# Optimization experiments

Measured on AMD Instinct MI355X. Metric: run time of the kernel, lower is better.

Reference implementation:

```python
import jax, jax.numpy as jnp
import numpy as np

N = 100000      # nodes (dtype==2 subgraph)
E = 1600000     # edges
IN_DIM = 256
OUT_DIM = 64
FEAT_DIM = 64   # hard-coded by nn.Linear(64, out_dim) in dstfeat_fc


def setup_inputs() -> dict:
    key = jax.random.key(0)
    k1, k2, k3, k4, k5, k6 = jax.random.split(key, 6)
    h = jax.random.normal(k1, (N, IN_DIM), dtype=jnp.float32)
    feat = jax.random.normal(k2, (N, FEAT_DIM), dtype=jnp.float32)
    W_fc = jax.random.normal(k3, (OUT_DIM, IN_DIM), dtype=jnp.float32) * 0.05
    W_dst = jax.random.normal(k4, (OUT_DIM, FEAT_DIM), dtype=jnp.float32) * 0.05
    src = jax.random.randint(k5, (E,), 0, N, dtype=jnp.int64)
    dst = jax.random.randint(k6, (E,), 0, N, dtype=jnp.int64)
    return {"h": h, "feat": feat, "W_fc": W_fc, "W_dst": W_dst, "src": src, "dst": dst}


def reference(h, feat, W_fc, W_dst, src, dst):
    # node projections (done once per node, then gathered per edge)
    z = h @ W_fc.T            # [N, OUT]  (self.fc)
    df = feat @ W_dst.T       # [N, OUT]  (self.dstfeat_fc on dst 'feat')

    # per-edge attention logit: dot(z[src], dstfeat[dst])
    e = jnp.sum(z[src] * df[dst], axis=-1)          # [E]

    # segment softmax over incoming edges of each destination node
    emax = jax.ops.segment_max(e, dst, num_segments=N)
    emax = jnp.where(jnp.isfinite(emax), emax, 0.0)  # guard empty segments
    ex = jnp.exp(e - emax[dst])                      # [E]
    denom = jax.ops.segment_sum(ex, dst, num_segments=N)  # [N]

    # weighted neighbor aggregation: sum_e alpha_e * z[src_e] per dst
    num = jax.ops.segment_sum(ex[:, None] * z[src], dst, num_segments=N)  # [N, OUT]
    out = num / jnp.where(denom == 0, 1.0, denom)[:, None]
    return out
```

## Files before the change

### kernel.cpp

```cpp
#include <hip/hip_runtime.h>
#include <math.h>

typedef unsigned int uint32;
typedef __attribute__((ext_vector_type(8))) short bf16x8;
typedef __attribute__((ext_vector_type(4))) float f32x4;

__device__ __forceinline__ ushort f2bf(float f) {
  uint32 u = __builtin_bit_cast(uint32, f);
  uint32 r = (u + 0x7fff + ((u >> 16) & 1)) >> 16;
  return (ushort)r;
}
__device__ __forceinline__ float bf_lo(uint32 u) {
  return __builtin_bit_cast(float, u << 16);
}
__device__ __forceinline__ float bf_hi(uint32 u) {
  return __builtin_bit_cast(float, u & 0xffff0000u);
}

template <bool BF16OUT>
__global__ __launch_bounds__(256) void gemm_mfma(const float* __restrict__ A,
                                                 const float* __restrict__ W,
                                                 float* __restrict__ C,
                                                 ushort* __restrict__ Cb,
                                                 int M, int K) {
  __shared__ __align__(16) ushort Ws[64 * 264];
  __shared__ __align__(16) ushort As[128 * 40];
  const int t = threadIdx.x;
  const int lane = t & 63;
  const int w = t >> 6;
  const int quad = lane >> 4;
  const int l16 = lane & 15;
  const int rBase = blockIdx.x * 128;

  const int kq4 = K >> 2;
  for (int idx = t; idx < 64 * kq4; idx += 256) {
    int row = idx / kq4, kq = idx - row * kq4;
    float4 v = *(const float4*)(W + (size_t)row * K + kq * 4);
    ushort4 b;
    b.x = f2bf(v.x); b.y = f2bf(v.y); b.z = f2bf(v.z); b.w = f2bf(v.w);
    *(ushort4*)&Ws[row * 264 + kq * 4] = b;
  }

  f32x4 acc[2][4];
  #pragma unroll
  for (int i = 0; i < 2; ++i)
    #pragma unroll
    for (int n = 0; n < 4; ++n) acc[i][n] = (f32x4){0.f, 0.f, 0.f, 0.f};

  const int rStage = t >> 1;
  const int halfStage = t & 1;

  for (int kb = 0; kb < K; kb += 32) {
    {
      int gr = rBase + rStage;
      #pragma unroll
      for (int q = 0; q < 4; ++q) {
        int kk = kb + halfStage * 16 + q * 4;
        float4 v = make_float4(0.f, 0.f, 0.f, 0.f);
        if (gr < M) v = *(const float4*)(A + (size_t)gr * K + kk);
        ushort4 b;
        b.x = f2bf(v.x); b.y = f2bf(v.y); b.z = f2bf(v.z); b.w = f2bf(v.w);
        *(ushort4*)&As[rStage * 40 + halfStage * 16 + q * 4] = b;
      }
    }
    __syncthreads();

    bf16x8 afrag[2], bfrag[4];
    #pragma unroll
    for (int i = 0; i < 2; ++i)
      afrag[i] = *(const bf16x8*)&As[(w * 32 + i * 16 + l16) * 40 + quad * 8];
    #pragma unroll
    for (int n = 0; n < 4; ++n)
      bfrag[n] = *(const bf16x8*)&Ws[(n * 16 + l16) * 264 + kb + quad * 8];

    #pragma unroll
    for (int i = 0; i < 2; ++i)
      #pragma unroll
      for (int n = 0; n < 4; ++n)
        acc[i][n] = __builtin_amdgcn_mfma_f32_16x16x32_bf16(afrag[i], bfrag[n],
                                                            acc[i][n], 0, 0, 0);
    __syncthreads();
  }

  #pragma unroll
  for (int i = 0; i < 2; ++i)
    #pragma unroll
    for (int nt = 0; nt < 4; ++nt)
      #pragma unroll
      for (int r = 0; r < 4; ++r) {
        int row = rBase + w * 32 + i * 16 + quad * 4 + r;
        int col = nt * 16 + l16;
        if (row < M) {
          if (BF16OUT)
            Cb[(size_t)row * 64 + col] = f2bf(acc[i][nt][r]);
          else
            C[(size_t)row * 64 + col] = acc[i][nt][r];
        }
      }
}

#define BBITS 7
#define BNODES 128
#define P_CHUNK 16384
#define P3_CAP 6144
#define MAXB 1024

__global__ __launch_bounds__(256) void bucket_count(const int* __restrict__ dst,
                                                    int* __restrict__ bucketCnt,
                                                    int E, int B) {
  __shared__ int lcnt[MAXB];
  const int t = threadIdx.x;
  for (int i = t; i < B; i += 256) lcnt[i] = 0;
  __syncthreads();
  int c0 = blockIdx.x * P_CHUNK, c1 = min(c0 + P_CHUNK, E);
  for (int i = c0 + t; i < c1; i += 256) atomicAdd(&lcnt[dst[i] >> BBITS], 1);
  __syncthreads();
  for (int b = t; b < B; b += 256) {
    int c = lcnt[b];
    if (c) atomicAdd(&bucketCnt[b], c);
  }
}

__global__ __launch_bounds__(1024) void bucket_scan(const int* __restrict__ bucketCnt,
                                                    int* __restrict__ bucketBase,
                                                    int* __restrict__ bucketCursor,
                                                    int* __restrict__ offsets,
                                                    int B, int N, int E) {
  __shared__ int waveSums[16];
  const int t = threadIdx.x;
  const int lane = t & 63, wave = t >> 6;
  int x = (t < B) ? bucketCnt[t] : 0;
  int inc = x;
  #pragma unroll
  for (int d = 1; d < 64; d <<= 1) {
    int o = __shfl_up(inc, d, 64);
    if (lane >= d) inc += o;
  }
  if (lane == 63) waveSums[wave] = inc;
  __syncthreads();
  int wbase = 0;
  #pragma unroll
  for (int w = 0; w < 16; ++w)
    if (w < wave) wbase += waveSums[w];
  int excl = wbase + inc - x;
  if (t < B) {
    bucketBase[t] = excl;
    bucketCursor[t] = excl;
  }
  if (t == 0) {
    bucketBase[B] = E;
    offsets[N] = E;
  }
}

__global__ __launch_bounds__(256) void bucket_partition(const int* __restrict__ src,
                                                        const int* __restrict__ dst,
                                                        int* __restrict__ bucketCursor,
                                                        unsigned* __restrict__ packed,
                                                        int E, int B) {
  __shared__ int lcnt[MAXB];
  __shared__ int lbase[MAXB];
  const int t = threadIdx.x;
  for (int i = t; i < B; i += 256) lcnt[i] = 0;
  __syncthreads();
  int c0 = blockIdx.x * P_CHUNK, c1 = min(c0 + P_CHUNK, E);
  for (int i = c0 + t; i < c1; i += 256) atomicAdd(&lcnt[dst[i] >> BBITS], 1);
  __syncthreads();
  for (int b = t; b < B; b += 256) {
    int c = lcnt[b];
    lbase[b] = c ? atomicAdd(&bucketCursor[b], c) : 0;
  }
  __syncthreads();
  for (int i = c0 + t; i < c1; i += 256) {
    int dv = dst[i];
    int b = dv >> BBITS;
    int pos = atomicAdd(&lbase[b], 1);
    packed[pos] = ((unsigned)src[i] << BBITS) | (unsigned)(dv & (BNODES - 1));
  }
}

__global__ __launch_bounds__(256) void bucket_finalize(const int* __restrict__ bucketBase,
                                                       unsigned* __restrict__ packed,
                                                       int* __restrict__ offsets, int N) {
  __shared__ unsigned stage[P3_CAP];
  __shared__ int cnt[BNODES];
  const int b = blockIdx.x;
  const int t = threadIdx.x;
  const int base = bucketBase[b];
  int n = bucketBase[b + 1] - base;
  if (n > P3_CAP) n = P3_CAP;
  for (int i = t; i < n; i += 256) stage[i] = packed[base + i];
  if (t < BNODES) cnt[t] = 0;
  __syncthreads();
  for (int i = t; i < n; i += 256) atomicAdd(&cnt[stage[i] & (BNODES - 1)], 1);
  __syncthreads();
  if (t < 64) {
    int cA = cnt[2 * t], cB = cnt[2 * t + 1];
    int s = cA + cB;
    int inc = s;
    #pragma unroll
    for (int d = 1; d < 64; d <<= 1) {
      int o = __shfl_up(inc, d, 64);
      if (t >= d) inc += o;
    }
    int excl = inc - s;
    cnt[2 * t] = base + excl;
    cnt[2 * t + 1] = base + excl + cA;
  }
  __syncthreads();
  const int node0 = b << BBITS;
  if (t < BNODES) {
    int g = node0 + t;
    if (g < N) offsets[g] = cnt[t];
  }
  __syncthreads();
  for (int i = t; i < n; i += 256) {
    unsigned v = stage[i];
    int pos = atomicAdd(&cnt[v & (BNODES - 1)], 1);
    packed[pos] = v >> BBITS;
  }
}

__global__ __launch_bounds__(256) void aggregate(const ushort* __restrict__ zb,
                                                 const float* __restrict__ df,
                                                 const int* __restrict__ offsets,
                                                 const int* __restrict__ edgeSrc,
                                                 float* __restrict__ out, int N) {
  int gwave = (blockIdx.x * blockDim.x + threadIdx.x) >> 6;
  int lane = threadIdx.x & 63;
  if (gwave >= N) return;
  const int d = __builtin_amdgcn_readfirstlane(gwave);
  const int g = lane >> 4;
  const int l16 = lane & 15;
  const int beg = offsets[d];
  const int end = offsets[d + 1];

  const float4 df4 = *(const float4*)(df + (size_t)d * 64 + l16 * 4);

  float m = -INFINITY, l = 0.f;
  float ax = 0.f, ay = 0.f, az = 0.f, aw = 0.f;

  for (int j0 = beg; j0 < end; j0 += 32) {
    const int nst = min(8, (end - j0 + 3) >> 2);
    uint2 zf[8];
    float ew[8];
    float bm = -INFINITY;

    #pragma unroll
    for (int st = 0; st < 8; ++st) {
      if (st < nst) {
        const int eidx = j0 + st * 4 + g;
        const bool act = eidx < end;
        int s = 0;
        if (act) s = edgeSrc[eidx];
        zf[st] = *(const uint2*)(zb + (size_t)s * 64 + l16 * 4);
        float p = bf_lo(zf[st].x) * df4.x;
        p = fmaf(bf_hi(zf[st].x), df4.y, p);
        p = fmaf(bf_lo(zf[st].y), df4.z, p);
        p = fmaf(bf_hi(zf[st].y), df4.w, p);
        p += __shfl_xor(p, 1, 64);
        p += __shfl_xor(p, 2, 64);
        p += __shfl_xor(p, 4, 64);
        p += __shfl_xor(p, 8, 64);
        ew[st] = act ? p : -INFINITY;
        bm = fmaxf(bm, ew[st]);
      }
    }
    bm = fmaxf(bm, __shfl_xor(bm, 16, 64));
    bm = fmaxf(bm, __shfl_xor(bm, 32, 64));

    const float nm = fmaxf(m, bm);
    const float alpha = __expf(m - nm);
    float sw = 0.f;
    #pragma unroll
    for (int st = 0; st < 8; ++st) {
      if (st < nst) {
        const float w = __expf(ew[st] - nm);
        ew[st] = w;
        sw += w;
      }
    }
    sw += __shfl_xor(sw, 16, 64);
    sw += __shfl_xor(sw, 32, 64);
    l = l * alpha + sw;
    m = nm;

    ax *= alpha; ay *= alpha; az *= alpha; aw *= alpha;
    #pragma unroll
    for (int st = 0; st < 8; ++st) {
      if (st < nst) {
        const float w = ew[st];
        ax = fmaf(w, bf_lo(zf[st].x), ax);
        ay = fmaf(w, bf_hi(zf[st].x), ay);
        az = fmaf(w, bf_lo(zf[st].y), az);
        aw = fmaf(w, bf_hi(zf[st].y), aw);
      }
    }
  }

  ax += __shfl_xor(ax, 16, 64); ax += __shfl_xor(ax, 32, 64);
  ay += __shfl_xor(ay, 16, 64); ay += __shfl_xor(ay, 32, 64);
  az += __shfl_xor(az, 16, 64); az += __shfl_xor(az, 32, 64);
  aw += __shfl_xor(aw, 16, 64); aw += __shfl_xor(aw, 32, 64);

  if (lane < 16) {
    const float inv = (l > 0.f) ? (1.f / l) : 0.f;
    float4 o;
    o.x = ax * inv; o.y = ay * inv; o.z = az * inv; o.w = aw * inv;
    *(float4*)(out + (size_t)d * 64 + l16 * 4) = o;
  }
}

extern "C" void kernel_launch(void* const* d_in, const int* in_sizes, int n_in,
                              void* d_out, int out_size, void* d_ws, size_t ws_size,
                              hipStream_t stream) {
  const float* h     = (const float*)d_in[0];
  const float* feat  = (const float*)d_in[1];
  const float* W_fc  = (const float*)d_in[2];
  const float* W_dst = (const float*)d_in[3];
  const int*   src   = (const int*)d_in[4];
  const int*   dst   = (const int*)d_in[5];
  float* out = (float*)d_out;

  const int N = in_sizes[1] / 64;
  const int E = in_sizes[4];
  const int IN_DIM = in_sizes[0] / N;
  const int FEAT_DIM = 64;
  const int B = (N + BNODES - 1) >> BBITS;

  char* ws = (char*)d_ws;
  ushort* zb = (ushort*)ws;
  float* df = (float*)(zb + (size_t)N * 64);
  int* offsets = (int*)(df + (size_t)N * 64);
  unsigned* packed = (unsigned*)(offsets + N + 1);
  int* bucketCnt = (int*)(packed + E);
  int* bucketBase = bucketCnt + B;
  int* bucketCursor = bucketBase + B + 1;

  hipMemsetAsync(bucketCnt, 0, sizeof(int) * (size_t)B, stream);

  int ggrid = (N + 127) / 128;
  gemm_mfma<true><<<ggrid, 256, 0, stream>>>(h, W_fc, nullptr, zb, N, IN_DIM);
  gemm_mfma<false><<<ggrid, 256, 0, stream>>>(feat, W_dst, df, nullptr, N, FEAT_DIM);

  int pgrid = (E + P_CHUNK - 1) / P_CHUNK;
  bucket_count<<<pgrid, 256, 0, stream>>>(dst, bucketCnt, E, B);
  bucket_scan<<<1, 1024, 0, stream>>>(bucketCnt, bucketBase, bucketCursor, offsets, B, N, E);
  bucket_partition<<<pgrid, 256, 0, stream>>>(src, dst, bucketCursor, packed, E, B);
  bucket_finalize<<<B, 256, 0, stream>>>(bucketBase, packed, offsets, N);

  aggregate<<<(N + 3) / 4, 256, 0, stream>>>(zb, df, offsets, (const int*)packed, out, N);
}
```

Baseline: 406.5 us.

## Replace two-level bucket sort CSR build with per-node atomic counting sort

Replaces the bucketed two-pass partition and finalize with a direct counting sort: global per-node degree atomics, a hierarchical three-kernel prefix scan, and a scatter that uses per-node atomic cursors. This drops the LDS staging and the second packed pass, but it puts 1.6M random global atomics in each of two kernels. It also adds kernel launches, and the order of edges within a node becomes nondeterministic. scan_top assumes nparts is at most 256.

```diff
diff --git a/kernel.cpp b/kernel.cpp
--- a/kernel.cpp
+++ b/kernel.cpp
@@ -99,126 +99,118 @@
       }
 }
 
-#define BBITS 7
-#define BNODES 128
-#define P_CHUNK 16384
-#define P3_CAP 6144
-#define MAXB 1024
-
-__global__ __launch_bounds__(256) void bucket_count(const int* __restrict__ dst,
-                                                    int* __restrict__ bucketCnt,
-                                                    int E, int B) {
-  __shared__ int lcnt[MAXB];
-  const int t = threadIdx.x;
-  for (int i = t; i < B; i += 256) lcnt[i] = 0;
-  __syncthreads();
-  int c0 = blockIdx.x * P_CHUNK, c1 = min(c0 + P_CHUNK, E);
-  for (int i = c0 + t; i < c1; i += 256) atomicAdd(&lcnt[dst[i] >> BBITS], 1);
-  __syncthreads();
-  for (int b = t; b < B; b += 256) {
-    int c = lcnt[b];
-    if (c) atomicAdd(&bucketCnt[b], c);
-  }
-}
-
-__global__ __launch_bounds__(1024) void bucket_scan(const int* __restrict__ bucketCnt,
-                                                    int* __restrict__ bucketBase,
-                                                    int* __restrict__ bucketCursor,
-                                                    int* __restrict__ offsets,
-                                                    int B, int N, int E) {
-  __shared__ int waveSums[16];
+__global__ __launch_bounds__(256) void deg_count(const int* __restrict__ dst,
+                                                 int* __restrict__ deg, int E) {
+  const int tid = blockIdx.x * blockDim.x + threadIdx.x;
+  const int stride = gridDim.x * blockDim.x;
+  const int E4 = E >> 2;
+  const int4* __restrict__ d4 = (const int4*)dst;
+  for (int i = tid; i < E4; i += stride) {
+    int4 v = d4[i];
+    atomicAdd(&deg[v.x], 1);
+    atomicAdd(&deg[v.y], 1);
+    atomicAdd(&deg[v.z], 1);
+    atomicAdd(&deg[v.w], 1);
+  }
+  for (int i = E4 * 4 + tid; i < E; i += stride) atomicAdd(&deg[dst[i]], 1);
+}
+
+__global__ __launch_bounds__(256) void scan_part(const int* __restrict__ deg,
+                                                 int* __restrict__ offsets,
+                                                 int* __restrict__ partials, int N) {
+  __shared__ int wsum[4];
   const int t = threadIdx.x;
   const int lane = t & 63, wave = t >> 6;
-  int x = (t < B) ? bucketCnt[t] : 0;
-  int inc = x;
+  const int i0 = blockIdx.x * 1024 + t * 4;
+  int v[4];
+  if (i0 + 3 < N) {
+    int4 x = *(const int4*)(deg + i0);
+    v[0] = x.x; v[1] = x.y; v[2] = x.z; v[3] = x.w;
+  } else {
+    #pragma unroll
+    for (int k = 0; k < 4; ++k) v[k] = (i0 + k < N) ? deg[i0 + k] : 0;
+  }
+  int s = v[0] + v[1] + v[2] + v[3];
+  int inc = s;
   #pragma unroll
   for (int d = 1; d < 64; d <<= 1) {
     int o = __shfl_up(inc, d, 64);
     if (lane >= d) inc += o;
   }
-  if (lane == 63) waveSums[wave] = inc;
+  if (lane == 63) wsum[wave] = inc;
   __syncthreads();
   int wbase = 0;
   #pragma unroll
-  for (int w = 0; w < 16; ++w)
-    if (w < wave) wbase += waveSums[w];
-  int excl = wbase + inc - x;
-  if (t < B) {
-    bucketBase[t] = excl;
-    bucketCursor[t] = excl;
-  }
-  if (t == 0) {
-    bucketBase[B] = E;
-    offsets[N] = E;
-  }
-}
-
-__global__ __launch_bounds__(256) void bucket_partition(const int* __restrict__ src,
-                                                        const int* __restrict__ dst,
-                                                        int* __restrict__ bucketCursor,
-                                                        unsigned* __restrict__ packed,
-                                                        int E, int B) {
-  __shared__ int lcnt[MAXB];
-  __shared__ int lbase[MAXB];
+  for (int w = 0; w < 4; ++w)
+    if (w < wave) wbase += wsum[w];
+  int run = wbase + inc - s;
+  if (i0 + 3 < N) {
+    int4 o;
+    o.x = run; o.y = run + v[0]; o.z = run + v[0] + v[1]; o.w = run + v[0] + v[1] + v[2];
+    *(int4*)(offsets + i0) = o;
+  } else {
+    #pragma unroll
+    for (int k = 0; k < 4; ++k) {
+      if (i0 + k < N) offsets[i0 + k] = run;
+      run += v[k];
+    }
+  }
+  if (t == 255) partials[blockIdx.x] = wbase + inc;
+}
+
+__global__ __launch_bounds__(256) void scan_top(int* __restrict__ partials,
+                                                int* __restrict__ offsets,
+                                                int nparts, int N, int E) {
+  __shared__ int wsum[4];
   const int t = threadIdx.x;
-  for (int i = t; i < B; i += 256) lcnt[i] = 0;
+  const int lane = t & 63, wave = t >> 6;
+  int x = (t < nparts) ? partials[t] : 0;
+  int inc = x;
+  #pragma unroll
+  for (int d = 1; d < 64; d <<= 1) {
+    int o = __shfl_up(inc, d, 64);
+    if (lane >= d) inc += o;
+  }
+  if (lane == 63) wsum[wave] = inc;
   __syncthreads();
-  int c0 = blockIdx.x * P_CHUNK, c1 = min(c0 + P_CHUNK, E);
-  for (int i = c0 + t; i < c1; i += 256) atomicAdd(&lcnt[dst[i] >> BBITS], 1);
-  __syncthreads();
-  for (int b = t; b < B; b += 256) {
-    int c = lcnt[b];
-    lbase[b] = c ? atomicAdd(&bucketCursor[b], c) : 0;
-  }
-  __syncthreads();
-  for (int i = c0 + t; i < c1; i += 256) {
-    int dv = dst[i];
-    int b = dv >> BBITS;
-    int pos = atomicAdd(&lbase[b], 1);
-    packed[pos] = ((unsigned)src[i] << BBITS) | (unsigned)(dv & (BNODES - 1));
-  }
-}
-
-__global__ __launch_bounds__(256) void bucket_finalize(const int* __restrict__ bucketBase,
-                                                       unsigned* __restrict__ packed,
-                                                       int* __restrict__ offsets, int N) {
-  __shared__ unsigned stage[P3_CAP];
-  __shared__ int cnt[BNODES];
-  const int b = blockIdx.x;
-  const int t = threadIdx.x;
-  const int base = bucketBase[b];
-  int n = bucketBase[b + 1] - base;
-  if (n > P3_CAP) n = P3_CAP;
-  for (int i = t; i < n; i += 256) stage[i] = packed[base + i];
-  if (t < BNODES) cnt[t] = 0;
-  __syncthreads();
-  for (int i = t; i < n; i += 256) atomicAdd(&cnt[stage[i] & (BNODES - 1)], 1);
-  __syncthreads();
-  if (t < 64) {
-    int cA = cnt[2 * t], cB = cnt[2 * t + 1];
-    int s = cA + cB;
-    int inc = s;
-    #pragma unroll
-    for (int d = 1; d < 64; d <<= 1) {
-      int o = __shfl_up(inc, d, 64);
-      if (t >= d) inc += o;
-    }
-    int excl = inc - s;
-    cnt[2 * t] = base + excl;
-    cnt[2 * t + 1] = base + excl + cA;
-  }
-  __syncthreads();
-  const int node0 = b << BBITS;
-  if (t < BNODES) {
-    int g = node0 + t;
-    if (g < N) offsets[g] = cnt[t];
-  }
-  __syncthreads();
-  for (int i = t; i < n; i += 256) {
-    unsigned v = stage[i];
-    int pos = atomicAdd(&cnt[v & (BNODES - 1)], 1);
-    packed[pos] = v >> BBITS;
-  }
+  int wbase = 0;
+  #pragma unroll
+  for (int w = 0; w < 4; ++w)
+    if (w < wave) wbase += wsum[w];
+  if (t < nparts) partials[t] = wbase + inc - x;
+  if (t == 0) offsets[N] = E;
+}
+
+__global__ __launch_bounds__(256) void scan_add(int* __restrict__ offsets,
+                                                const int* __restrict__ partials,
+                                                int* __restrict__ cursor, int N) {
+  const int i = blockIdx.x * blockDim.x + threadIdx.x;
+  if (i < N) {
+    int v = offsets[i] + partials[i >> 10];
+    offsets[i] = v;
+    cursor[i] = v;
+  }
+}
+
+__global__ __launch_bounds__(256) void scatter(const int* __restrict__ src,
+                                               const int* __restrict__ dst,
+                                               int* __restrict__ cursor,
+                                               int* __restrict__ edgeSrc, int E) {
+  const int tid = blockIdx.x * blockDim.x + threadIdx.x;
+  const int stride = gridDim.x * blockDim.x;
+  const int E4 = E >> 2;
+  const int4* __restrict__ d4 = (const int4*)dst;
+  const int4* __restrict__ s4 = (const int4*)src;
+  for (int i = tid; i < E4; i += stride) {
+    int4 dv = d4[i];
+    int4 sv = s4[i];
+    edgeSrc[atomicAdd(&cursor[dv.x], 1)] = sv.x;
+    edgeSrc[atomicAdd(&cursor[dv.y], 1)] = sv.y;
+    edgeSrc[atomicAdd(&cursor[dv.z], 1)] = sv.z;
+    edgeSrc[atomicAdd(&cursor[dv.w], 1)] = sv.w;
+  }
+  for (int i = E4 * 4 + tid; i < E; i += stride)
+    edgeSrc[atomicAdd(&cursor[dst[i]], 1)] = src[i];
 }
 
 __global__ __launch_bounds__(256) void aggregate(const ushort* __restrict__ zb,
@@ -325,29 +317,27 @@
   const int N = in_sizes[1] / 64;
   const int E = in_sizes[4];
   const int IN_DIM = in_sizes[0] / N;
-  const int FEAT_DIM = 64;
-  const int B = (N + BNODES - 1) >> BBITS;
 
   char* ws = (char*)d_ws;
   ushort* zb = (ushort*)ws;
   float* df = (float*)(zb + (size_t)N * 64);
-  int* offsets = (int*)(df + (size_t)N * 64);
-  unsigned* packed = (unsigned*)(offsets + N + 1);
-  int* bucketCnt = (int*)(packed + E);
-  int* bucketBase = bucketCnt + B;
-  int* bucketCursor = bucketBase + B + 1;
-
-  hipMemsetAsync(bucketCnt, 0, sizeof(int) * (size_t)B, stream);
+  int* deg = (int*)(df + (size_t)N * 64);
+  int* offsets = deg + N;
+  int* edgeSrc = offsets + N + 1;
+  int* partials = edgeSrc + E;
+
+  hipMemsetAsync(deg, 0, sizeof(int) * (size_t)N, stream);
 
   int ggrid = (N + 127) / 128;
   gemm_mfma<true><<<ggrid, 256, 0, stream>>>(h, W_fc, nullptr, zb, N, IN_DIM);
-  gemm_mfma<false><<<ggrid, 256, 0, stream>>>(feat, W_dst, df, nullptr, N, FEAT_DIM);
-
-  int pgrid = (E + P_CHUNK - 1) / P_CHUNK;
-  bucket_count<<<pgrid, 256, 0, stream>>>(dst, bucketCnt, E, B);
-  bucket_scan<<<1, 1024, 0, stream>>>(bucketCnt, bucketBase, bucketCursor, offsets, B, N, E);
-  bucket_partition<<<pgrid, 256, 0, stream>>>(src, dst, bucketCursor, packed, E, B);
-  bucket_finalize<<<B, 256, 0, stream>>>(bucketBase, packed, offsets, N);
-
-  aggregate<<<(N + 3) / 4, 256, 0, stream>>>(zb, df, offsets, (const int*)packed, out, N);
-}
+  gemm_mfma<false><<<ggrid, 256, 0, stream>>>(feat, W_dst, df, nullptr, N, 64);
+
+  const int nparts = (N + 1023) / 1024;
+  deg_count<<<1024, 256, 0, stream>>>(dst, deg, E);
+  scan_part<<<nparts, 256, 0, stream>>>(deg, offsets, partials, N);
+  scan_top<<<1, 256, 0, stream>>>(partials, offsets, nparts, N, E);
+  scan_add<<<(N + 255) / 256, 256, 0, stream>>>(offsets, partials, deg, N);
+  scatter<<<1024, 256, 0, stream>>>(src, dst, deg, edgeSrc, E);
+
+  aggregate<<<(N + 3) / 4, 256, 0, stream>>>(zb, df, offsets, edgeSrc, out, N);
+}
```

Measured after the change: 480.0 us. 18.1% more time.

## Replace single-pass bucket partition with coarse-then-fine two-level radix partition

Applied to the files above, without the earlier changes.

The CSR build now partitions edges by destination in two levels. A first pass scatters into about 49 coarse buckets, a middle pass splits each coarse bucket into 16 fine buckets, and a finalize pass sorts within each node. This replaces the single scatter into roughly 782 buckets, which had poorly coalesced writes and heavy global atomic traffic. It also uses smaller chunks (2048 edges) so more blocks run in parallel, and borrows the output buffer as scratch. The cost is an extra kernel launch and an extra full pass over the edge array.

```diff
diff --git a/kernel.cpp b/kernel.cpp
--- a/kernel.cpp
+++ b/kernel.cpp
@@ -99,37 +99,41 @@
       }
 }
 
-#define BBITS 7
-#define BNODES 128
-#define P_CHUNK 16384
+#define FBITS 7
+#define FNODES 128
+#define CBITS 11
+#define CH 2048
+#define S4_CAP 4096
 #define P3_CAP 6144
-#define MAXB 1024
-
-__global__ __launch_bounds__(256) void bucket_count(const int* __restrict__ dst,
-                                                    int* __restrict__ bucketCnt,
-                                                    int E, int B) {
-  __shared__ int lcnt[MAXB];
-  const int t = threadIdx.x;
-  for (int i = t; i < B; i += 256) lcnt[i] = 0;
-  __syncthreads();
-  int c0 = blockIdx.x * P_CHUNK, c1 = min(c0 + P_CHUNK, E);
-  for (int i = c0 + t; i < c1; i += 256) atomicAdd(&lcnt[dst[i] >> BBITS], 1);
-  __syncthreads();
-  for (int b = t; b < B; b += 256) {
+
+__global__ __launch_bounds__(256) void fine_count(const int* __restrict__ dst,
+                                                  int* __restrict__ fineCnt,
+                                                  int E, int Bf) {
+  __shared__ int lcnt[1024];
+  const int t = threadIdx.x;
+  for (int i = t; i < Bf; i += 256) lcnt[i] = 0;
+  __syncthreads();
+  int c0 = blockIdx.x * CH, c1 = min(c0 + CH, E);
+  for (int i = c0 + t; i < c1; i += 256) atomicAdd(&lcnt[dst[i] >> FBITS], 1);
+  __syncthreads();
+  for (int b = t; b < Bf; b += 256) {
     int c = lcnt[b];
-    if (c) atomicAdd(&bucketCnt[b], c);
-  }
-}
-
-__global__ __launch_bounds__(1024) void bucket_scan(const int* __restrict__ bucketCnt,
-                                                    int* __restrict__ bucketBase,
-                                                    int* __restrict__ bucketCursor,
-                                                    int* __restrict__ offsets,
-                                                    int B, int N, int E) {
+    if (c) atomicAdd(&fineCnt[b], c);
+  }
+}
+
+__global__ __launch_bounds__(1024) void scan_fine(const int* __restrict__ fineCnt,
+                                                  int* __restrict__ fineBase,
+                                                  int* __restrict__ fineCursor,
+                                                  int* __restrict__ coarseBase,
+                                                  int* __restrict__ coarseCursor,
+                                                  int* __restrict__ offsets,
+                                                  int Bf, int NC, int N, int E) {
   __shared__ int waveSums[16];
+  __shared__ int sExcl[1024];
   const int t = threadIdx.x;
   const int lane = t & 63, wave = t >> 6;
-  int x = (t < B) ? bucketCnt[t] : 0;
+  int x = (t < Bf) ? fineCnt[t] : 0;
   int inc = x;
   #pragma unroll
   for (int d = 1; d < 64; d <<= 1) {
@@ -143,56 +147,106 @@
   for (int w = 0; w < 16; ++w)
     if (w < wave) wbase += waveSums[w];
   int excl = wbase + inc - x;
-  if (t < B) {
-    bucketBase[t] = excl;
-    bucketCursor[t] = excl;
+  sExcl[t] = excl;
+  if (t < Bf) {
+    fineBase[t] = excl;
+    fineCursor[t] = excl;
   }
   if (t == 0) {
-    bucketBase[B] = E;
+    fineBase[Bf] = E;
     offsets[N] = E;
-  }
-}
-
-__global__ __launch_bounds__(256) void bucket_partition(const int* __restrict__ src,
+    coarseBase[NC] = E;
+  }
+  __syncthreads();
+  if (t < NC) {
+    int v = sExcl[t * 16];
+    coarseBase[t] = v;
+    coarseCursor[t] = v;
+  }
+}
+
+__global__ __launch_bounds__(256) void coarse_partition(const int* __restrict__ src,
                                                         const int* __restrict__ dst,
-                                                        int* __restrict__ bucketCursor,
-                                                        unsigned* __restrict__ packed,
-                                                        int E, int B) {
-  __shared__ int lcnt[MAXB];
-  __shared__ int lbase[MAXB];
-  const int t = threadIdx.x;
-  for (int i = t; i < B; i += 256) lcnt[i] = 0;
-  __syncthreads();
-  int c0 = blockIdx.x * P_CHUNK, c1 = min(c0 + P_CHUNK, E);
-  for (int i = c0 + t; i < c1; i += 256) atomicAdd(&lcnt[dst[i] >> BBITS], 1);
-  __syncthreads();
-  for (int b = t; b < B; b += 256) {
-    int c = lcnt[b];
-    lbase[b] = c ? atomicAdd(&bucketCursor[b], c) : 0;
+                                                        int* __restrict__ coarseCursor,
+                                                        unsigned* __restrict__ packedA,
+                                                        int E, int NC) {
+  __shared__ int lcnt[64];
+  __shared__ int lbase[64];
+  const int t = threadIdx.x;
+  if (t < NC) lcnt[t] = 0;
+  __syncthreads();
+  int c0 = blockIdx.x * CH, c1 = min(c0 + CH, E);
+  for (int i = c0 + t; i < c1; i += 256) atomicAdd(&lcnt[dst[i] >> CBITS], 1);
+  __syncthreads();
+  if (t < NC) {
+    int c = lcnt[t];
+    lbase[t] = c ? atomicAdd(&coarseCursor[t], c) : 0;
   }
   __syncthreads();
   for (int i = c0 + t; i < c1; i += 256) {
     int dv = dst[i];
-    int b = dv >> BBITS;
+    int b = dv >> CBITS;
     int pos = atomicAdd(&lbase[b], 1);
-    packed[pos] = ((unsigned)src[i] << BBITS) | (unsigned)(dv & (BNODES - 1));
-  }
-}
-
-__global__ __launch_bounds__(256) void bucket_finalize(const int* __restrict__ bucketBase,
-                                                       unsigned* __restrict__ packed,
-                                                       int* __restrict__ offsets, int N) {
+    packedA[pos] = ((unsigned)src[i] << CBITS) | (unsigned)(dv & ((1 << CBITS) - 1));
+  }
+}
+
+__global__ __launch_bounds__(256) void mid_partition(const unsigned* __restrict__ packedA,
+                                                     const int* __restrict__ coarseBase,
+                                                     int* __restrict__ fineCursor,
+                                                     unsigned* __restrict__ packedB) {
+  __shared__ unsigned stage[S4_CAP];
+  __shared__ int cnt[16];
+  __shared__ int lbase[16];
+  const int cb = blockIdx.x >> 4;
+  const int sub = blockIdx.x & 15;
+  const int t = threadIdx.x;
+  const int base = coarseBase[cb];
+  const int endr = coarseBase[cb + 1];
+  const int len = endr - base;
+  const int chunk = (len + 15) >> 4;
+  int s0 = base + sub * chunk;
+  int s1 = min(s0 + chunk, endr);
+  for (int p0 = s0; p0 < s1; p0 += S4_CAP) {
+    const int n = min(S4_CAP, s1 - p0);
+    if (t < 16) cnt[t] = 0;
+    __syncthreads();
+    for (int i = t; i < n; i += 256) {
+      unsigned v = packedA[p0 + i];
+      stage[i] = v;
+      atomicAdd(&cnt[(v >> FBITS) & 15], 1);
+    }
+    __syncthreads();
+    if (t < 16) {
+      int c = cnt[t];
+      lbase[t] = c ? atomicAdd(&fineCursor[cb * 16 + t], c) : 0;
+    }
+    __syncthreads();
+    for (int i = t; i < n; i += 256) {
+      unsigned v = stage[i];
+      int f = (v >> FBITS) & 15;
+      int pos = atomicAdd(&lbase[f], 1);
+      packedB[pos] = ((v >> CBITS) << FBITS) | (v & (FNODES - 1));
+    }
+    __syncthreads();
+  }
+}
+
+__global__ __launch_bounds__(256) void fine_finalize(const int* __restrict__ fineBase,
+                                                     const unsigned* __restrict__ packedB,
+                                                     int* __restrict__ edgeSrc,
+                                                     int* __restrict__ offsets, int N) {
   __shared__ unsigned stage[P3_CAP];
-  __shared__ int cnt[BNODES];
+  __shared__ int cnt[FNODES];
   const int b = blockIdx.x;
   const int t = threadIdx.x;
-  const int base = bucketBase[b];
-  int n = bucketBase[b + 1] - base;
+  const int base = fineBase[b];
+  int n = fineBase[b + 1] - base;
   if (n > P3_CAP) n = P3_CAP;
-  for (int i = t; i < n; i += 256) stage[i] = packed[base + i];
-  if (t < BNODES) cnt[t] = 0;
-  __syncthreads();
-  for (int i = t; i < n; i += 256) atomicAdd(&cnt[stage[i] & (BNODES - 1)], 1);
+  for (int i = t; i < n; i += 256) stage[i] = packedB[base + i];
+  if (t < FNODES) cnt[t] = 0;
+  __syncthreads();
+  for (int i = t; i < n; i += 256) atomicAdd(&cnt[stage[i] & (FNODES - 1)], 1);
   __syncthreads();
   if (t < 64) {
     int cA = cnt[2 * t], cB = cnt[2 * t + 1];
@@ -208,16 +262,16 @@
     cnt[2 * t + 1] = base + excl + cA;
   }
   __syncthreads();
-  const int node0 = b << BBITS;
-  if (t < BNODES) {
+  const int node0 = b << FBITS;
+  if (t < FNODES) {
     int g = node0 + t;
     if (g < N) offsets[g] = cnt[t];
   }
   __syncthreads();
   for (int i = t; i < n; i += 256) {
     unsigned v = stage[i];
-    int pos = atomicAdd(&cnt[v & (BNODES - 1)], 1);
-    packed[pos] = v >> BBITS;
+    int pos = atomicAdd(&cnt[v & (FNODES - 1)], 1);
+    edgeSrc[pos] = (int)(v >> FBITS);
   }
 }
 
@@ -325,29 +379,35 @@
   const int N = in_sizes[1] / 64;
   const int E = in_sizes[4];
   const int IN_DIM = in_sizes[0] / N;
-  const int FEAT_DIM = 64;
-  const int B = (N + BNODES - 1) >> BBITS;
+
+  const int Bf = (N + FNODES - 1) >> FBITS;
+  const int NC = (Bf + 15) >> 4;
 
   char* ws = (char*)d_ws;
   ushort* zb = (ushort*)ws;
   float* df = (float*)(zb + (size_t)N * 64);
   int* offsets = (int*)(df + (size_t)N * 64);
-  unsigned* packed = (unsigned*)(offsets + N + 1);
-  int* bucketCnt = (int*)(packed + E);
-  int* bucketBase = bucketCnt + B;
-  int* bucketCursor = bucketBase + B + 1;
-
-  hipMemsetAsync(bucketCnt, 0, sizeof(int) * (size_t)B, stream);
+  unsigned* packedA = (unsigned*)(offsets + N + 1);
+  int* fineCnt = (int*)(packedA + E);
+  int* fineBase = fineCnt + Bf;
+  int* fineCursor = fineBase + Bf + 1;
+  int* coarseBase = fineCursor + Bf;
+  int* coarseCursor = coarseBase + NC + 1;
+  unsigned* packedB = (unsigned*)d_out;
+
+  hipMemsetAsync(fineCnt, 0, sizeof(int) * (size_t)Bf, stream);
 
   int ggrid = (N + 127) / 128;
   gemm_mfma<true><<<ggrid, 256, 0, stream>>>(h, W_fc, nullptr, zb, N, IN_DIM);
-  gemm_mfma<false><<<ggrid, 256, 0, stream>>>(feat, W_dst, df, nullptr, N, FEAT_DIM);
-
-  int pgrid = (E + P_CHUNK - 1) / P_CHUNK;
-  bucket_count<<<pgrid, 256, 0, stream>>>(dst, bucketCnt, E, B);
-  bucket_scan<<<1, 1024, 0, stream>>>(bucketCnt, bucketBase, bucketCursor, offsets, B, N, E);
-  bucket_partition<<<pgrid, 256, 0, stream>>>(src, dst, bucketCursor, packed, E, B);
-  bucket_finalize<<<B, 256, 0, stream>>>(bucketBase, packed, offsets, N);
-
-  aggregate<<<(N + 3) / 4, 256, 0, stream>>>(zb, df, offsets, (const int*)packed, out, N);
-}
+  gemm_mfma<false><<<ggrid, 256, 0, stream>>>(feat, W_dst, df, nullptr, N, 64);
+
+  const int pgrid = (E + CH - 1) / CH;
+  fine_count<<<pgrid, 256, 0, stream>>>(dst, fineCnt, E, Bf);
+  scan_fine<<<1, 1024, 0, stream>>>(fineCnt, fineBase, fineCursor, coarseBase,
+                                    coarseCursor, offsets, Bf, NC, N, E);
+  coarse_partition<<<pgrid, 256, 0, stream>>>(src, dst, coarseCursor, packedA, E, NC);
+  mid_partition<<<NC * 16, 256, 0, stream>>>(packedA, coarseBase, fineCursor, packedB);
+  fine_finalize<<<Bf, 256, 0, stream>>>(fineBase, packedB, (int*)packedA, offsets, N);
+
+  aggregate<<<(N + 3) / 4, 256, 0, stream>>>(zb, df, offsets, (const int*)packedA, out, N);
+}
```

New measurement: 371.8 us. -8.5%, faster.

## Merge projection GEMMs and restructure CSR build with larger buckets

Applied to the files above, without the earlier changes.

Fuses the two projection GEMMs into one launch by splitting the grid between the h and feat paths. The CSR bucketing moves to 512-node buckets with smaller 4096-edge chunks, so there are more partition blocks. The finalize step now reads packed entries straight from global memory instead of staging them in shared memory with a cap, and writes into a separate edgeSrc array. The output buffer is reused as scratch for the packed array. This removes one launch and the shared-memory capacity limit, at the cost of more global atomic traffic per block and uncached reads in finalize.

```diff
diff --git a/kernel.cpp b/kernel.cpp
--- a/kernel.cpp
+++ b/kernel.cpp
@@ -17,20 +17,27 @@
   return __builtin_bit_cast(float, u & 0xffff0000u);
 }
 
-template <bool BF16OUT>
-__global__ __launch_bounds__(256) void gemm_mfma(const float* __restrict__ A,
-                                                 const float* __restrict__ W,
-                                                 float* __restrict__ C,
-                                                 ushort* __restrict__ Cb,
-                                                 int M, int K) {
+__global__ __launch_bounds__(256) void gemm_both(const float* __restrict__ h,
+                                                 const float* __restrict__ feat,
+                                                 const float* __restrict__ W_fc,
+                                                 const float* __restrict__ W_dst,
+                                                 ushort* __restrict__ zb,
+                                                 float* __restrict__ df,
+                                                 int M, int gsplit) {
   __shared__ __align__(16) ushort Ws[64 * 264];
   __shared__ __align__(16) ushort As[128 * 40];
+  const bool second = (int)blockIdx.x >= gsplit;
+  const float* __restrict__ A = second ? feat : h;
+  const float* __restrict__ W = second ? W_dst : W_fc;
+  const int K = second ? 64 : 256;
+  const int bx = second ? (int)blockIdx.x - gsplit : (int)blockIdx.x;
+
   const int t = threadIdx.x;
   const int lane = t & 63;
   const int w = t >> 6;
   const int quad = lane >> 4;
   const int l16 = lane & 15;
-  const int rBase = blockIdx.x * 128;
+  const int rBase = bx * 128;
 
   const int kq4 = K >> 2;
   for (int idx = t; idx < 64 * kq4; idx += 256) {
@@ -91,133 +98,138 @@
         int row = rBase + w * 32 + i * 16 + quad * 4 + r;
         int col = nt * 16 + l16;
         if (row < M) {
-          if (BF16OUT)
-            Cb[(size_t)row * 64 + col] = f2bf(acc[i][nt][r]);
+          if (!second)
+            zb[(size_t)row * 64 + col] = f2bf(acc[i][nt][r]);
           else
-            C[(size_t)row * 64 + col] = acc[i][nt][r];
+            df[(size_t)row * 64 + col] = acc[i][nt][r];
         }
       }
 }
 
-#define BBITS 7
-#define BNODES 128
-#define P_CHUNK 16384
-#define P3_CAP 6144
-#define MAXB 1024
-
-__global__ __launch_bounds__(256) void bucket_count(const int* __restrict__ dst,
-                                                    int* __restrict__ bucketCnt,
-                                                    int E, int B) {
-  __shared__ int lcnt[MAXB];
-  const int t = threadIdx.x;
-  for (int i = t; i < B; i += 256) lcnt[i] = 0;
-  __syncthreads();
-  int c0 = blockIdx.x * P_CHUNK, c1 = min(c0 + P_CHUNK, E);
-  for (int i = c0 + t; i < c1; i += 256) atomicAdd(&lcnt[dst[i] >> BBITS], 1);
-  __syncthreads();
-  for (int b = t; b < B; b += 256) {
-    int c = lcnt[b];
-    if (c) atomicAdd(&bucketCnt[b], c);
-  }
-}
-
-__global__ __launch_bounds__(1024) void bucket_scan(const int* __restrict__ bucketCnt,
-                                                    int* __restrict__ bucketBase,
-                                                    int* __restrict__ bucketCursor,
-                                                    int* __restrict__ offsets,
-                                                    int B, int N, int E) {
-  __shared__ int waveSums[16];
+#define NBBITS 9
+#define BKNODES 512
+#define CH 4096
+#define NBMAX 256
+
+__global__ __launch_bounds__(256) void csr_count(const int* __restrict__ dst,
+                                                 int* __restrict__ bCnt, int E, int NB) {
+  __shared__ int lcnt[NBMAX];
+  const int t = threadIdx.x;
+  if (t < NB) lcnt[t] = 0;
+  __syncthreads();
+  const int c0 = blockIdx.x * CH, c1 = min(c0 + CH, E);
+  for (int i = c0 + t; i < c1; i += 256) atomicAdd(&lcnt[dst[i] >> NBBITS], 1);
+  __syncthreads();
+  if (t < NB) {
+    int c = lcnt[t];
+    if (c) atomicAdd(&bCnt[t], c);
+  }
+}
+
+__global__ __launch_bounds__(256) void csr_scan(const int* __restrict__ bCnt,
+                                                int* __restrict__ bBase,
+                                                int* __restrict__ bCursor,
+                                                int* __restrict__ offsets,
+                                                int NB, int N, int E) {
+  __shared__ int wsum[4];
   const int t = threadIdx.x;
   const int lane = t & 63, wave = t >> 6;
-  int x = (t < B) ? bucketCnt[t] : 0;
+  int x = (t < NB) ? bCnt[t] : 0;
   int inc = x;
   #pragma unroll
   for (int d = 1; d < 64; d <<= 1) {
     int o = __shfl_up(inc, d, 64);
     if (lane >= d) inc += o;
   }
-  if (lane == 63) waveSums[wave] = inc;
+  if (lane == 63) wsum[wave] = inc;
   __syncthreads();
   int wbase = 0;
   #pragma unroll
-  for (int w = 0; w < 16; ++w)
-    if (w < wave) wbase += waveSums[w];
+  for (int w = 0; w < 4; ++w)
+    if (w < wave) wbase += wsum[w];
   int excl = wbase + inc - x;
-  if (t < B) {
-    bucketBase[t] = excl;
-    bucketCursor[t] = excl;
+  if (t < NB) {
+    bBase[t] = excl;
+    bCursor[t] = excl;
   }
   if (t == 0) {
-    bucketBase[B] = E;
+    bBase[NB] = E;
     offsets[N] = E;
   }
 }
 
-__global__ __launch_bounds__(256) void bucket_partition(const int* __restrict__ src,
-                                                        const int* __restrict__ dst,
-                                                        int* __restrict__ bucketCursor,
-                                                        unsigned* __restrict__ packed,
-                                                        int E, int B) {
-  __shared__ int lcnt[MAXB];
-  __shared__ int lbase[MAXB];
-  const int t = threadIdx.x;
-  for (int i = t; i < B; i += 256) lcnt[i] = 0;
-  __syncthreads();
-  int c0 = blockIdx.x * P_CHUNK, c1 = min(c0 + P_CHUNK, E);
-  for (int i = c0 + t; i < c1; i += 256) atomicAdd(&lcnt[dst[i] >> BBITS], 1);
-  __syncthreads();
-  for (int b = t; b < B; b += 256) {
-    int c = lcnt[b];
-    lbase[b] = c ? atomicAdd(&bucketCursor[b], c) : 0;
+__global__ __launch_bounds__(256) void csr_partition(const int* __restrict__ src,
+                                                     const int* __restrict__ dst,
+                                                     int* __restrict__ bCursor,
+                                                     unsigned* __restrict__ packed,
+                                                     int E, int NB) {
+  __shared__ int lcnt[NBMAX];
+  __shared__ int lbase[NBMAX];
+  const int t = threadIdx.x;
+  if (t < NB) lcnt[t] = 0;
+  __syncthreads();
+  const int c0 = blockIdx.x * CH, c1 = min(c0 + CH, E);
+  for (int i = c0 + t; i < c1; i += 256) atomicAdd(&lcnt[dst[i] >> NBBITS], 1);
+  __syncthreads();
+  if (t < NB) {
+    int c = lcnt[t];
+    lbase[t] = c ? atomicAdd(&bCursor[t], c) : 0;
   }
   __syncthreads();
   for (int i = c0 + t; i < c1; i += 256) {
     int dv = dst[i];
-    int b = dv >> BBITS;
+    int b = dv >> NBBITS;
     int pos = atomicAdd(&lbase[b], 1);
-    packed[pos] = ((unsigned)src[i] << BBITS) | (unsigned)(dv & (BNODES - 1));
-  }
-}
-
-__global__ __launch_bounds__(256) void bucket_finalize(const int* __restrict__ bucketBase,
-                                                       unsigned* __restrict__ packed,
-                                                       int* __restrict__ offsets, int N) {
-  __shared__ unsigned stage[P3_CAP];
-  __shared__ int cnt[BNODES];
-  const int b = blockIdx.x;
-  const int t = threadIdx.x;
-  const int base = bucketBase[b];
-  int n = bucketBase[b + 1] - base;
-  if (n > P3_CAP) n = P3_CAP;
-  for (int i = t; i < n; i += 256) stage[i] = packed[base + i];
-  if (t < BNODES) cnt[t] = 0;
-  __syncthreads();
-  for (int i = t; i < n; i += 256) atomicAdd(&cnt[stage[i] & (BNODES - 1)], 1);
-  __syncthreads();
-  if (t < 64) {
-    int cA = cnt[2 * t], cB = cnt[2 * t + 1];
+    packed[pos] = ((unsigned)src[i] << NBBITS) | (unsigned)(dv & (BKNODES - 1));
+  }
+}
+
+__global__ __launch_bounds__(256) void csr_finalize(const int* __restrict__ bBase,
+                                                    const unsigned* __restrict__ packed,
+                                                    int* __restrict__ edgeSrc,
+                                                    int* __restrict__ offsets, int N) {
+  __shared__ int sh[BKNODES];
+  __shared__ int wsum[4];
+  const int r = blockIdx.x;
+  const int t = threadIdx.x;
+  const int lane = t & 63, wave = t >> 6;
+  const int base = bBase[r];
+  const int endr = bBase[r + 1];
+  for (int i = t; i < BKNODES; i += 256) sh[i] = 0;
+  __syncthreads();
+  for (int i = base + t; i < endr; i += 256)
+    atomicAdd(&sh[packed[i] & (BKNODES - 1)], 1);
+  __syncthreads();
+  {
+    int cA = sh[2 * t], cB = sh[2 * t + 1];
     int s = cA + cB;
     int inc = s;
     #pragma unroll
     for (int d = 1; d < 64; d <<= 1) {
       int o = __shfl_up(inc, d, 64);
-      if (t >= d) inc += o;
-    }
-    int excl = inc - s;
-    cnt[2 * t] = base + excl;
-    cnt[2 * t + 1] = base + excl + cA;
-  }
-  __syncthreads();
-  const int node0 = b << BBITS;
-  if (t < BNODES) {
-    int g = node0 + t;
-    if (g < N) offsets[g] = cnt[t];
-  }
-  __syncthreads();
-  for (int i = t; i < n; i += 256) {
-    unsigned v = stage[i];
-    int pos = atomicAdd(&cnt[v & (BNODES - 1)], 1);
-    packed[pos] = v >> BBITS;
+      if (lane >= d) inc += o;
+    }
+    if (lane == 63) wsum[wave] = inc;
+    __syncthreads();
+    int wbase = 0;
+    #pragma unroll
+    for (int w = 0; w < 4; ++w)
+      if (w < wave) wbase += wsum[w];
+    int excl = wbase + inc - s;
+    sh[2 * t] = base + excl;
+    sh[2 * t + 1] = base + excl + cA;
+  }
+  __syncthreads();
+  const int node0 = r << NBBITS;
+  for (int k = t; k < BKNODES; k += 256) {
+    int g = node0 + k;
+    if (g < N) offsets[g] = sh[k];
+  }
+  __syncthreads();
+  for (int i = base + t; i < endr; i += 256) {
+    unsigned v = packed[i];
+    int pos = atomicAdd(&sh[v & (BKNODES - 1)], 1);
+    edgeSrc[pos] = (int)(v >> NBBITS);
   }
 }
 
@@ -324,30 +336,29 @@
 
   const int N = in_sizes[1] / 64;
   const int E = in_sizes[4];
-  const int IN_DIM = in_sizes[0] / N;
-  const int FEAT_DIM = 64;
-  const int B = (N + BNODES - 1) >> BBITS;
+
+  const int NB = (N + BKNODES - 1) >> NBBITS;
+  const int nChunks = (E + CH - 1) / CH;
 
   char* ws = (char*)d_ws;
   ushort* zb = (ushort*)ws;
   float* df = (float*)(zb + (size_t)N * 64);
   int* offsets = (int*)(df + (size_t)N * 64);
-  unsigned* packed = (unsigned*)(offsets + N + 1);
-  int* bucketCnt = (int*)(packed + E);
-  int* bucketBase = bucketCnt + B;
-  int* bucketCursor = bucketBase + B + 1;
-
-  hipMemsetAsync(bucketCnt, 0, sizeof(int) * (size_t)B, stream);
-
-  int ggrid = (N + 127) / 128;
-  gemm_mfma<true><<<ggrid, 256, 0, stream>>>(h, W_fc, nullptr, zb, N, IN_DIM);
-  gemm_mfma<false><<<ggrid, 256, 0, stream>>>(feat, W_dst, df, nullptr, N, FEAT_DIM);
-
-  int pgrid = (E + P_CHUNK - 1) / P_CHUNK;
-  bucket_count<<<pgrid, 256, 0, stream>>>(dst, bucketCnt, E, B);
-  bucket_scan<<<1, 1024, 0, stream>>>(bucketCnt, bucketBase, bucketCursor, offsets, B, N, E);
-  bucket_partition<<<pgrid, 256, 0, stream>>>(src, dst, bucketCursor, packed, E, B);
-  bucket_finalize<<<B, 256, 0, stream>>>(bucketBase, packed, offsets, N);
-
-  aggregate<<<(N + 3) / 4, 256, 0, stream>>>(zb, df, offsets, (const int*)packed, out, N);
-}
+  int* edgeSrc = offsets + N + 1;
+  int* bCnt = edgeSrc + E;
+  int* bBase = bCnt + NB;
+  int* bCursor = bBase + NB + 1;
+  unsigned* packed = (unsigned*)d_out;
+
+  hipMemsetAsync(bCnt, 0, sizeof(int) * (size_t)NB, stream);
+
+  const int gsplit = (N + 127) / 128;
+  gemm_both<<<gsplit * 2, 256, 0, stream>>>(h, feat, W_fc, W_dst, zb, df, N, gsplit);
+
+  csr_count<<<nChunks, 256, 0, stream>>>(dst, bCnt, E, NB);
+  csr_scan<<<1, 256, 0, stream>>>(bCnt, bBase, bCursor, offsets, NB, N, E);
+  csr_partition<<<nChunks, 256, 0, stream>>>(src, dst, bCursor, packed, E, NB);
+  csr_finalize<<<NB, 256, 0, stream>>>(bBase, packed, edgeSrc, offsets, N);
+
+  aggregate<<<(N + 3) / 4, 256, 0, stream>>>(zb, df, offsets, edgeSrc, out, N);
+}
```

Result: faster. 358.2 us (-11.9%).
